# Kernel optimization log

Hardware: AMD Instinct MI355X
Metric: run time of the kernel (lower is better)

Reference implementation:

```python
import jax, jax.numpy as jnp
import numpy as np
from jax import lax

D = 1024
K = 3
LN_EPS = 1e-5


def setup_inputs() -> dict:
    key = jax.random.key(0)
    ks = jax.random.split(key, 8)
    B, T = 8, 4096
    x = jax.random.normal(ks[0], (B, T, D), dtype=jnp.float32)
    s = 1.0 / np.sqrt(D)
    in_proj_w = jax.random.uniform(ks[1], (D, 2 * D), jnp.float32, -s, s)
    in_proj_b = jax.random.uniform(ks[2], (2 * D,), jnp.float32, -s, s)
    conv_w = jax.random.uniform(ks[3], (D, 1, K), jnp.float32, -1.0 / np.sqrt(K), 1.0 / np.sqrt(K))
    conv_b = jax.random.uniform(ks[4], (D,), jnp.float32, -1.0 / np.sqrt(K), 1.0 / np.sqrt(K))
    logit_a = jnp.zeros((D,), jnp.float32)
    ssm_b = jnp.full((D,), 0.1, jnp.float32)
    ssm_c = jnp.ones((D,), jnp.float32)
    ssm_d = jnp.zeros((D,), jnp.float32)
    out_proj_w = jax.random.uniform(ks[5], (D, D), jnp.float32, -s, s)
    out_proj_b = jax.random.uniform(ks[6], (D,), jnp.float32, -s, s)
    ln_w = jnp.ones((D,), jnp.float32)
    ln_b = jnp.zeros((D,), jnp.float32)
    return {"x": x, "in_proj_w": in_proj_w, "in_proj_b": in_proj_b,
            "conv_w": conv_w, "conv_b": conv_b, "logit_a": logit_a,
            "ssm_b": ssm_b, "ssm_c": ssm_c, "ssm_d": ssm_d,
            "out_proj_w": out_proj_w, "out_proj_b": out_proj_b,
            "ln_w": ln_w, "ln_b": ln_b}


def _dwconv(v, conv_w, conv_b):
    # v: (B, T, D) -> depthwise conv1d, kernel K, 'same' padding
    vt = jnp.transpose(v, (0, 2, 1))  # (B, D, T)
    out = lax.conv_general_dilated(
        vt, conv_w, window_strides=(1,), padding=[(K // 2, K // 2)],
        dimension_numbers=("NCH", "OIH", "NCH"), feature_group_count=D)
    out = out + conv_b[None, :, None]
    return jnp.transpose(out, (0, 2, 1))  # (B, T, D)


def reference(x, in_proj_w, in_proj_b, conv_w, conv_b, logit_a,
              ssm_b, ssm_c, ssm_d, out_proj_w, out_proj_b, ln_w, ln_b):
    B, T, _ = x.shape
    residual = x
    uv = x @ in_proj_w + in_proj_b                      # (B, T, 2D)
    u, v = uv[..., :D], uv[..., D:]
    v = jax.nn.silu(v)
    v_local = _dwconv(v, conv_w, conv_b)                # (B, T, D)

    a = jax.nn.sigmoid(logit_a).astype(v_local.dtype)
    # diagonal LTI scan: h_t = a*h_{t-1} + b*u_t ; y_t = c*h_t + d*u_t
    def step(h, vt):
        h = a * h + ssm_b * vt
        return h, ssm_c * h + ssm_d * vt
    h0 = jnp.zeros((B, D), v_local.dtype)
    _, y_seq = lax.scan(step, h0, jnp.transpose(v_local, (1, 0, 2)))
    y_seq = jnp.transpose(y_seq, (1, 0, 2))             # (B, T, D)

    out = u * jax.nn.silu(y_seq)
    out = out @ out_proj_w + out_proj_b                 # dropout: eval mode (identity)
    h = out + residual
    mu = jnp.mean(h, axis=-1, keepdims=True)
    var = jnp.mean(jnp.square(h - mu), axis=-1, keepdims=True)
    return (h - mu) * lax.rsqrt(var + LN_EPS) * ln_w + ln_b
```

## Files before the change

kernel.cpp:

```cpp
#include <hip/hip_runtime.h>
#include <cstdint>
#include <cstddef>

#define D_DIM   1024
#define TWO_D   2048
#define B_DIM   8
#define T_DIM   4096
#define BT_DIM  (B_DIM*T_DIM)
#define LN_EPS  1e-5f
#define NCHUNK  128
#define CLEN    (T_DIM/NCHUNK)

typedef __attribute__((ext_vector_type(8))) short bf16x8;
typedef __attribute__((ext_vector_type(4))) float f32x4;

__device__ __forceinline__ float bf2f(unsigned short u){
  union { unsigned int i; float f; } c; c.i = ((unsigned int)u) << 16; return c.f;
}
__device__ __forceinline__ unsigned short f2bf(float f){
  union { float f; unsigned int i; } c; c.f = f;
  unsigned int x = c.i;
  return (unsigned short)((x + 0x7fffu + ((x >> 16) & 1u)) >> 16);
}
__device__ __forceinline__ float sigmoidf_(float x){ return 1.f/(1.f+__expf(-x)); }
__device__ __forceinline__ float siluf_(float x){ return x/(1.f+__expf(-x)); }


__global__ void cvt_f32_bf16(const float* __restrict__ in, unsigned short* __restrict__ out, int n){
  int i = (blockIdx.x*blockDim.x + threadIdx.x)*4;
  const int stride = gridDim.x*blockDim.x*4;
  for (; i + 3 < n; i += stride){
    float4 f = *(const float4*)(in + i);
    ushort4 o; o.x=f2bf(f.x); o.y=f2bf(f.y); o.z=f2bf(f.z); o.w=f2bf(f.w);
    *(ushort4*)(out + i) = o;
  }
}

__global__ void cvt_transpose(const float* __restrict__ W, unsigned short* __restrict__ Wt,
                              int rows, int cols){
  int i = blockIdx.x*blockDim.x + threadIdx.x;
  const int total = rows*cols;
  const int stride = gridDim.x*blockDim.x;
  for (; i < total; i += stride){
    int n = i / rows, k = i % rows;
    Wt[i] = f2bf(W[(size_t)k*cols + n]);
  }
}

template<int EPI>
__global__ __launch_bounds__(512, 2) void gemm256(
    const unsigned short* __restrict__ A,
    const unsigned short* __restrict__ Bt,
    const float* __restrict__ bias,
    const float* __restrict__ resid,
    unsigned short* __restrict__ outU,
    unsigned short* __restrict__ outV,
    float* __restrict__ outF,
    const int K, const int nbn)
{
  __shared__ __align__(16) unsigned short sA[2][2][8192];
  __shared__ __align__(16) unsigned short sB[2][2][8192];

#define BARRIER()   __builtin_amdgcn_s_barrier()
#define FENCE()     __builtin_amdgcn_sched_barrier(0)
#define WAIT_VM4()  do { asm volatile("s_waitcnt vmcnt(4)"); FENCE(); } while(0)
#define WAIT_VM0()  do { asm volatile("s_waitcnt vmcnt(0)"); FENCE(); } while(0)

  const int tid  = threadIdx.x;
  const int lane = tid & 63;
  const int wv   = tid >> 6;
  const int wr   = wv >> 2;
  const int wc   = wv & 3;
  const int fr   = lane & 15;
  const int fq   = lane >> 4;

  const int nwg = gridDim.x;
  const int cpx = nwg >> 3;
  const int wg  = (blockIdx.x & 7) * cpx + (blockIdx.x >> 3);
  const int bm = wg / nbn, bn = wg % nbn;

  const unsigned short* Ag = A  + (size_t)bm * 256 * K;
  const unsigned short* Bg = Bt + (size_t)bn * 256 * K;

  const int r0  = tid >> 2;
  const int r1  = 128 + r0;
  const int c0  = tid & 3;
  const int cs0 = c0 ^ ((r0 >> 1) & 3);
  const int cs1 = c0 ^ ((r1 >> 1) & 3);
  const int ld0 = tid * 8;
  const int ld1 = (512 + tid) * 8;

#define STAGE(ARR, srcp, kofs)                                                           \
  do {                                                                                   \
    __builtin_amdgcn_global_load_lds(                                                    \
      (const __attribute__((address_space(1))) void*)((srcp) + (size_t)r0*K + (kofs) + cs0*8), \
      (__attribute__((address_space(3))) void*)(&(ARR)[ld0]), 16, 0, 0);                 \
    __builtin_amdgcn_global_load_lds(                                                    \
      (const __attribute__((address_space(1))) void*)((srcp) + (size_t)r1*K + (kofs) + cs1*8), \
      (__attribute__((address_space(3))) void*)(&(ARR)[ld1]), 16, 0, 0);                 \
  } while(0)

  const int swz  = fq ^ ((fr >> 1) & 3);
  const int offA = (wr*128 + fr) * 32 + swz * 8;
  const int offB = (wc*64  + fr) * 32 + swz * 8;

  f32x4 acc[8][4];
#pragma unroll
  for (int i = 0; i < 8; ++i)
#pragma unroll
    for (int j = 0; j < 4; ++j) acc[i][j] = {0.f,0.f,0.f,0.f};

  bf16x8 afr[4], bfr[4];

#define PHASE(PAR, KH, MH, STAGE_STMT, TAIL_WAIT)                          \
  do {                                                                     \
    _Pragma("unroll")                                                      \
    for (int m2 = 0; m2 < 4; ++m2)                                         \
      afr[m2] = *(const bf16x8*)(&sA[PAR][KH][offA + ((MH)*4+m2)*512]);    \
    if ((MH) == 0) {                                                       \
      _Pragma("unroll")                                                    \
      for (int n2 = 0; n2 < 4; ++n2)                                       \
        bfr[n2] = *(const bf16x8*)(&sB[PAR][KH][offB + n2*512]);           \
    }                                                                      \
    STAGE_STMT;                                                            \
    BARRIER();                                                             \
    asm volatile("s_waitcnt lgkmcnt(0)");                                  \
    FENCE();                                                               \
    __builtin_amdgcn_s_setprio(1);                                         \
    _Pragma("unroll")                                                      \
    for (int n2 = 0; n2 < 4; ++n2)                                         \
      _Pragma("unroll")                                                    \
      for (int m2 = 0; m2 < 4; ++m2)                                       \
        acc[(MH)*4+m2][n2] = __builtin_amdgcn_mfma_f32_16x16x32_bf16(      \
            afr[m2], bfr[n2], acc[(MH)*4+m2][n2], 0, 0, 0);                \
    __builtin_amdgcn_s_setprio(0);                                         \
    TAIL_WAIT;                                                             \
    BARRIER();                                                             \
  } while(0)

  const int npairs = K >> 7;

  STAGE(sA[0][0], Ag, 0);
  STAGE(sB[0][0], Bg, 0);
  STAGE(sA[0][1], Ag, 32);
  STAGE(sB[0][1], Bg, 32);
  WAIT_VM4();
  BARRIER();

  for (int i = 0; i < npairs - 1; ++i){
    const int kbO = ((i << 1) + 1) << 6;
    const int kbE = ((i << 1) + 2) << 6;
    PHASE(0, 0, 0, STAGE(sA[1][0], Ag, kbO),      );
    PHASE(0, 0, 1, STAGE(sB[1][0], Bg, kbO),      WAIT_VM4());
    PHASE(0, 1, 0, STAGE(sA[1][1], Ag, kbO + 32), );
    PHASE(0, 1, 1, STAGE(sB[1][1], Bg, kbO + 32), WAIT_VM4());
    PHASE(1, 0, 0, STAGE(sA[0][0], Ag, kbE),      );
    PHASE(1, 0, 1, STAGE(sB[0][0], Bg, kbE),      WAIT_VM4());
    PHASE(1, 1, 0, STAGE(sA[0][1], Ag, kbE + 32), );
    PHASE(1, 1, 1, STAGE(sB[0][1], Bg, kbE + 32), WAIT_VM4());
  }
  PHASE(0, 0, 0, STAGE(sA[1][0], Ag, K - 64), );
  PHASE(0, 0, 1, STAGE(sB[1][0], Bg, K - 64), WAIT_VM4());
  PHASE(0, 1, 0, STAGE(sA[1][1], Ag, K - 32), );
  PHASE(0, 1, 1, STAGE(sB[1][1], Bg, K - 32), WAIT_VM4());
  PHASE(1, 0, 0, , );
  PHASE(1, 0, 1, , WAIT_VM0());
  PHASE(1, 1, 0, , );
  PHASE(1, 1, 1, , );

  const int nb = bn*256 + wc*64;
  const int mb = bm*256 + wr*128;
  float bsv[4];
#pragma unroll
  for (int ni = 0; ni < 4; ++ni) bsv[ni] = bias[nb + ni*16 + fr];

  if (EPI == 0){
    const bool isV = (nb >= D_DIM);
    unsigned short* dst = isV ? (outV + (nb - D_DIM)) : (outU + nb);
#pragma unroll
    for (int mi = 0; mi < 8; ++mi){
#pragma unroll
      for (int j = 0; j < 4; ++j){
        const int m = mb + mi*16 + fq*4 + j;
        unsigned short* row = dst + (size_t)m*D_DIM + fr;
#pragma unroll
        for (int ni = 0; ni < 4; ++ni){
          float cv = acc[mi][ni][j] + bsv[ni];
          row[ni*16] = f2bf(isV ? siluf_(cv) : cv);
        }
      }
    }
  } else {
#pragma unroll
    for (int mi = 0; mi < 8; ++mi){
#pragma unroll
      for (int j = 0; j < 4; ++j){
        const int m = mb + mi*16 + fq*4 + j;
        const float* rrow = resid + (size_t)m*D_DIM + nb + fr;
        float* orow = outF + (size_t)m*D_DIM + nb + fr;
#pragma unroll
        for (int ni = 0; ni < 4; ++ni)
          orow[ni*16] = acc[mi][ni][j] + bsv[ni] + rrow[ni*16];
      }
    }
  }
#undef PHASE
#undef STAGE
#undef BARRIER
#undef FENCE
#undef WAIT_VM4
#undef WAIT_VM0
}

__global__ __launch_bounds__(256) void scan_a(
    const unsigned short* __restrict__ v,
    const float* __restrict__ conv_w, const float* __restrict__ conv_b,
    const float* __restrict__ logit_a, const float* __restrict__ ssm_b,
    float* __restrict__ hend)
{
  const int b = blockIdx.x / NCHUNK;
  const int c = blockIdx.x % NCHUNK;
  const int d0 = threadIdx.x * 4;
  const int t0 = c * CLEN;
  const unsigned short* vb = v + (size_t)b * T_DIM * D_DIM;

  float w0[4], w1[4], w2[4], av[4], bv[4], cb[4];
#pragma unroll
  for (int i=0;i<4;i++){
    w0[i] = conv_w[(d0+i)*3+0];
    w1[i] = conv_w[(d0+i)*3+1];
    w2[i] = conv_w[(d0+i)*3+2];
    cb[i] = conv_b[d0+i];
    av[i] = sigmoidf_(logit_a[d0+i]);
    bv[i] = ssm_b[d0+i];
  }
  float vm1[4], v0[4], h[4] = {0.f,0.f,0.f,0.f};
  if (t0 == 0){
#pragma unroll
    for (int i=0;i<4;i++) vm1[i]=0.f;
  } else {
    ushort4 u = *(const ushort4*)(vb + (size_t)(t0-1)*D_DIM + d0);
    vm1[0]=bf2f(u.x); vm1[1]=bf2f(u.y); vm1[2]=bf2f(u.z); vm1[3]=bf2f(u.w);
  }
  {
    ushort4 u = *(const ushort4*)(vb + (size_t)t0*D_DIM + d0);
    v0[0]=bf2f(u.x); v0[1]=bf2f(u.y); v0[2]=bf2f(u.z); v0[3]=bf2f(u.w);
  }
#pragma unroll 8
  for (int t = t0; t < t0 + CLEN; ++t){
    float vp1[4];
    if (t + 1 < T_DIM){
      ushort4 u = *(const ushort4*)(vb + (size_t)(t+1)*D_DIM + d0);
      vp1[0]=bf2f(u.x); vp1[1]=bf2f(u.y); vp1[2]=bf2f(u.z); vp1[3]=bf2f(u.w);
    } else { vp1[0]=vp1[1]=vp1[2]=vp1[3]=0.f; }
#pragma unroll
    for (int i=0;i<4;i++){
      float vl = w0[i]*vm1[i] + w1[i]*v0[i] + w2[i]*vp1[i] + cb[i];
      h[i] = av[i]*h[i] + bv[i]*vl;
      vm1[i]=v0[i]; v0[i]=vp1[i];
    }
  }
  float* he = hend + ((size_t)b*NCHUNK + c)*D_DIM + d0;
#pragma unroll
  for (int i=0;i<4;i++) he[i] = h[i];
}

__global__ void scan_fix(const float* __restrict__ hend, const float* __restrict__ logit_a,
                         float* __restrict__ hinit)
{
  int idx = blockIdx.x*blockDim.x + threadIdx.x;
  if (idx >= B_DIM*D_DIM) return;
  const int b = idx / D_DIM, d = idx % D_DIM;
  const float a  = sigmoidf_(logit_a[d]);
  const float aL = __powf(a, (float)CLEN);
  float h = 0.f;
  for (int c = 0; c < NCHUNK; ++c){
    hinit[((size_t)b*NCHUNK + c)*D_DIM + d] = h;
    h = aL*h + hend[((size_t)b*NCHUNK + c)*D_DIM + d];
  }
}

__global__ __launch_bounds__(256) void scan_c(
    const unsigned short* __restrict__ v,
    const unsigned short* __restrict__ ubuf,
    const float* __restrict__ conv_w, const float* __restrict__ conv_b,
    const float* __restrict__ logit_a, const float* __restrict__ ssm_b,
    const float* __restrict__ ssm_c, const float* __restrict__ ssm_d,
    const float* __restrict__ hinit,
    unsigned short* __restrict__ gated)
{
  const int b = blockIdx.x / NCHUNK;
  const int c = blockIdx.x % NCHUNK;
  const int d0 = threadIdx.x * 4;
  const int t0 = c * CLEN;
  const unsigned short* vb = v    + (size_t)b * T_DIM * D_DIM;
  const unsigned short* ub = ubuf + (size_t)b * T_DIM * D_DIM;
  unsigned short* gb       = gated+ (size_t)b * T_DIM * D_DIM;

  float w0[4], w1[4], w2[4], av[4], bv[4], cb[4], scv[4], sdv[4], h[4];
#pragma unroll
  for (int i=0;i<4;i++){
    w0[i] = conv_w[(d0+i)*3+0];
    w1[i] = conv_w[(d0+i)*3+1];
    w2[i] = conv_w[(d0+i)*3+2];
    cb[i] = conv_b[d0+i];
    av[i] = sigmoidf_(logit_a[d0+i]);
    bv[i] = ssm_b[d0+i];
    scv[i] = ssm_c[d0+i];
    sdv[i] = ssm_d[d0+i];
    h[i] = hinit[((size_t)b*NCHUNK + c)*D_DIM + d0 + i];
  }
  float vm1[4], v0[4];
  if (t0 == 0){
#pragma unroll
    for (int i=0;i<4;i++) vm1[i]=0.f;
  } else {
    ushort4 u = *(const ushort4*)(vb + (size_t)(t0-1)*D_DIM + d0);
    vm1[0]=bf2f(u.x); vm1[1]=bf2f(u.y); vm1[2]=bf2f(u.z); vm1[3]=bf2f(u.w);
  }
  {
    ushort4 u = *(const ushort4*)(vb + (size_t)t0*D_DIM + d0);
    v0[0]=bf2f(u.x); v0[1]=bf2f(u.y); v0[2]=bf2f(u.z); v0[3]=bf2f(u.w);
  }
#pragma unroll 8
  for (int t = t0; t < t0 + CLEN; ++t){
    float vp1[4];
    if (t + 1 < T_DIM){
      ushort4 u = *(const ushort4*)(vb + (size_t)(t+1)*D_DIM + d0);
      vp1[0]=bf2f(u.x); vp1[1]=bf2f(u.y); vp1[2]=bf2f(u.z); vp1[3]=bf2f(u.w);
    } else { vp1[0]=vp1[1]=vp1[2]=vp1[3]=0.f; }
    ushort4 uu = *(const ushort4*)(ub + (size_t)t*D_DIM + d0);
    float uf[4] = { bf2f(uu.x), bf2f(uu.y), bf2f(uu.z), bf2f(uu.w) };
    ushort4 go;
    unsigned short gtmp[4];
#pragma unroll
    for (int i=0;i<4;i++){
      float vl = w0[i]*vm1[i] + w1[i]*v0[i] + w2[i]*vp1[i] + cb[i];
      h[i] = av[i]*h[i] + bv[i]*vl;
      float y = scv[i]*h[i] + sdv[i]*vl;
      gtmp[i] = f2bf(uf[i] * siluf_(y));
      vm1[i]=v0[i]; v0[i]=vp1[i];
    }
    go.x=gtmp[0]; go.y=gtmp[1]; go.z=gtmp[2]; go.w=gtmp[3];
    *(ushort4*)(gb + (size_t)t*D_DIM + d0) = go;
  }
}

__global__ __launch_bounds__(256) void ln_kernel(
    float* __restrict__ io, const float* __restrict__ lw, const float* __restrict__ lb)
{
  __shared__ float rs[4], rq[4];
  const int row = blockIdx.x;
  const int tid = threadIdx.x;
  float* p = io + (size_t)row * D_DIM;
  float4 x = *(const float4*)(p + tid*4);
  float s = x.x + x.y + x.z + x.w;
  float q = x.x*x.x + x.y*x.y + x.z*x.z + x.w*x.w;
#pragma unroll
  for (int off = 32; off > 0; off >>= 1){
    s += __shfl_down(s, off, 64);
    q += __shfl_down(q, off, 64);
  }
  const int wv = tid >> 6;
  if ((tid & 63) == 0){ rs[wv] = s; rq[wv] = q; }
  __syncthreads();
  const float ts = rs[0]+rs[1]+rs[2]+rs[3];
  const float tq = rq[0]+rq[1]+rq[2]+rq[3];
  const float mu  = ts * (1.f/(float)D_DIM);
  const float var = tq * (1.f/(float)D_DIM) - mu*mu;
  const float inv = rsqrtf(var + LN_EPS);
  const float4 w4 = *(const float4*)(lw + tid*4);
  const float4 b4 = *(const float4*)(lb + tid*4);
  float4 o;
  o.x = (x.x-mu)*inv*w4.x + b4.x;
  o.y = (x.y-mu)*inv*w4.y + b4.y;
  o.z = (x.z-mu)*inv*w4.z + b4.z;
  o.w = (x.w-mu)*inv*w4.w + b4.w;
  *(float4*)(p + tid*4) = o;
}

extern "C" void kernel_launch(void* const* d_in, const int* in_sizes, int n_in,
                              void* d_out, int out_size, void* d_ws, size_t ws_size,
                              hipStream_t stream)
{
  const float* x     = (const float*)d_in[0];
  const float* w1    = (const float*)d_in[1];
  const float* b1    = (const float*)d_in[2];
  const float* convw = (const float*)d_in[3];
  const float* convb = (const float*)d_in[4];
  const float* la    = (const float*)d_in[5];
  const float* sb    = (const float*)d_in[6];
  const float* sc    = (const float*)d_in[7];
  const float* sd    = (const float*)d_in[8];
  const float* w2    = (const float*)d_in[9];
  const float* b2    = (const float*)d_in[10];
  const float* lw    = (const float*)d_in[11];
  const float* lb    = (const float*)d_in[12];
  float* out = (float*)d_out;

  char* ws = (char*)d_ws;
  unsigned short* xb    = (unsigned short*)(ws + 0);
  unsigned short* ubf   = (unsigned short*)(ws + 67108864);
  unsigned short* vbf   = (unsigned short*)(ws + 134217728);
  unsigned short* w1t   = (unsigned short*)(ws + 201326592);
  unsigned short* w2t   = (unsigned short*)(ws + 205520896);
  float*          hend  = (float*)(ws + 207618048);
  float*          hinit = (float*)(ws + 211812352);

  cvt_f32_bf16<<<2048, 256, 0, stream>>>(x, xb, BT_DIM*D_DIM);
  cvt_transpose<<<2048, 256, 0, stream>>>(w1, w1t, D_DIM, TWO_D);
  cvt_transpose<<<1024, 256, 0, stream>>>(w2, w2t, D_DIM, D_DIM);

  gemm256<0><<<dim3((BT_DIM/256)*(TWO_D/256)), 512, 0, stream>>>(
      xb, w1t, b1, nullptr, ubf, vbf, nullptr, D_DIM, TWO_D/256);

  scan_a<<<B_DIM*NCHUNK, 256, 0, stream>>>(vbf, convw, convb, la, sb, hend);
  scan_fix<<<(B_DIM*D_DIM + 255)/256, 256, 0, stream>>>(hend, la, hinit);
  scan_c<<<B_DIM*NCHUNK, 256, 0, stream>>>(vbf, ubf, convw, convb, la, sb, sc, sd, hinit, xb);

  gemm256<1><<<dim3((BT_DIM/256)*(D_DIM/256)), 512, 0, stream>>>(
      xb, w2t, b2, x, nullptr, nullptr, out, D_DIM, D_DIM/256);

  ln_kernel<<<BT_DIM, 256, 0, stream>>>(out, lw, lb);
}
```

Measured before the change: 429.3 us.

## Double-buffer LDS fragment registers to overlap reads with MFMA in GEMM

```diff
diff --git a/kernel.cpp b/kernel.cpp
--- a/kernel.cpp
+++ b/kernel.cpp
@@ -63,8 +63,8 @@
 
 #define BARRIER()   __builtin_amdgcn_s_barrier()
 #define FENCE()     __builtin_amdgcn_sched_barrier(0)
-#define WAIT_VM4()  do { asm volatile("s_waitcnt vmcnt(4)"); FENCE(); } while(0)
-#define WAIT_VM0()  do { asm volatile("s_waitcnt vmcnt(0)"); FENCE(); } while(0)
+#define LGKM(N)     do { asm volatile("s_waitcnt lgkmcnt(" #N ")"); FENCE(); } while(0)
+#define VMW(N)      do { asm volatile("s_waitcnt vmcnt(" #N ")"); FENCE(); } while(0)
 
   const int tid  = threadIdx.x;
   const int lane = tid & 63;
@@ -90,7 +90,7 @@
   const int ld0 = tid * 8;
   const int ld1 = (512 + tid) * 8;
 
-#define STAGE(ARR, srcp, kofs)                                                           \
+#define STAGE1(ARR, srcp, kofs)                                                          \
   do {                                                                                   \
     __builtin_amdgcn_global_load_lds(                                                    \
       (const __attribute__((address_space(1))) void*)((srcp) + (size_t)r0*K + (kofs) + cs0*8), \
@@ -100,6 +100,14 @@
       (__attribute__((address_space(3))) void*)(&(ARR)[ld1]), 16, 0, 0);                 \
   } while(0)
 
+#define STAGE8(NP, kb)                 \
+  do {                                 \
+    STAGE1(sA[NP][0], Ag, (kb));       \
+    STAGE1(sB[NP][0], Bg, (kb));       \
+    STAGE1(sA[NP][1], Ag, (kb) + 32);  \
+    STAGE1(sB[NP][1], Bg, (kb) + 32);  \
+  } while(0)
+
   const int swz  = fq ^ ((fr >> 1) & 3);
   const int offA = (wr*128 + fr) * 32 + swz * 8;
   const int offB = (wc*64  + fr) * 32 + swz * 8;
@@ -110,63 +118,74 @@
 #pragma unroll
     for (int j = 0; j < 4; ++j) acc[i][j] = {0.f,0.f,0.f,0.f};
 
-  bf16x8 afr[4], bfr[4];
-
-#define PHASE(PAR, KH, MH, STAGE_STMT, TAIL_WAIT)                          \
+  bf16x8 afr[2][4], bfr[2][4];
+
+#define READ_A(SET, P, KH, MH)                                             \
+  do { _Pragma("unroll")                                                   \
+    for (int m2 = 0; m2 < 4; ++m2)                                         \
+      afr[SET][m2] = *(const bf16x8*)(&sA[P][KH][offA + ((MH)*4+m2)*512]); \
+  } while(0)
+#define READ_B(SET, P, KH)                                                 \
+  do { _Pragma("unroll")                                                   \
+    for (int n2 = 0; n2 < 4; ++n2)                                         \
+      bfr[SET][n2] = *(const bf16x8*)(&sB[P][KH][offB + n2*512]);          \
+  } while(0)
+#define MFMA16(AS, BS, ACB)                                                \
   do {                                                                     \
-    _Pragma("unroll")                                                      \
-    for (int m2 = 0; m2 < 4; ++m2)                                         \
-      afr[m2] = *(const bf16x8*)(&sA[PAR][KH][offA + ((MH)*4+m2)*512]);    \
-    if ((MH) == 0) {                                                       \
-      _Pragma("unroll")                                                    \
-      for (int n2 = 0; n2 < 4; ++n2)                                       \
-        bfr[n2] = *(const bf16x8*)(&sB[PAR][KH][offB + n2*512]);           \
-    }                                                                      \
-    STAGE_STMT;                                                            \
-    BARRIER();                                                             \
-    asm volatile("s_waitcnt lgkmcnt(0)");                                  \
-    FENCE();                                                               \
     __builtin_amdgcn_s_setprio(1);                                         \
     _Pragma("unroll")                                                      \
     for (int n2 = 0; n2 < 4; ++n2)                                         \
       _Pragma("unroll")                                                    \
       for (int m2 = 0; m2 < 4; ++m2)                                       \
-        acc[(MH)*4+m2][n2] = __builtin_amdgcn_mfma_f32_16x16x32_bf16(      \
-            afr[m2], bfr[n2], acc[(MH)*4+m2][n2], 0, 0, 0);                \
+        acc[(ACB)+m2][n2] = __builtin_amdgcn_mfma_f32_16x16x32_bf16(       \
+            afr[AS][m2], bfr[BS][n2], acc[(ACB)+m2][n2], 0, 0, 0);         \
     __builtin_amdgcn_s_setprio(0);                                         \
-    TAIL_WAIT;                                                             \
+  } while(0)
+
+#define TILE(P, NP, KB, LAST)                                              \
+  do {                                                                     \
+                 \
+    READ_A(1, P, 0, 1);                                                    \
+    if (!(LAST)) STAGE8(NP, KB);                                           \
+    FENCE(); BARRIER(); LGKM(4);                                           \
+    MFMA16(0, 0, 0);                                                       \
+    if (LAST) { VMW(0); } else { VMW(8); }              \
     BARRIER();                                                             \
+     \
+    READ_A(0, P, 1, 0); READ_B(1, P, 1);                                   \
+    FENCE(); BARRIER(); LGKM(8);                                           \
+    MFMA16(1, 0, 4);                                                       \
+    BARRIER();                                                             \
+                 \
+    READ_A(1, P, 1, 1);                                                    \
+    FENCE(); BARRIER(); LGKM(4);                                           \
+    MFMA16(0, 1, 0);                                                       \
+    if (!(LAST)) VMW(4);                              \
+    BARRIER();                                                             \
+     \
+    if (!(LAST)) { READ_A(0, NP, 0, 0); READ_B(0, NP, 0); }                \
+    FENCE(); BARRIER();                                                    \
+    if (LAST) { LGKM(0); } else { LGKM(8); }                               \
+    MFMA16(1, 1, 4);                                                       \
+    BARRIER();                                                             \
   } while(0)
 
   const int npairs = K >> 7;
 
-  STAGE(sA[0][0], Ag, 0);
-  STAGE(sB[0][0], Bg, 0);
-  STAGE(sA[0][1], Ag, 32);
-  STAGE(sB[0][1], Bg, 32);
-  WAIT_VM4();
+  STAGE8(0, 0);
+  VMW(4);
   BARRIER();
+  READ_A(0, 0, 0, 0); READ_B(0, 0, 0);
+  FENCE();
 
   for (int i = 0; i < npairs - 1; ++i){
     const int kbO = ((i << 1) + 1) << 6;
     const int kbE = ((i << 1) + 2) << 6;
-    PHASE(0, 0, 0, STAGE(sA[1][0], Ag, kbO),      );
-    PHASE(0, 0, 1, STAGE(sB[1][0], Bg, kbO),      WAIT_VM4());
-    PHASE(0, 1, 0, STAGE(sA[1][1], Ag, kbO + 32), );
-    PHASE(0, 1, 1, STAGE(sB[1][1], Bg, kbO + 32), WAIT_VM4());
-    PHASE(1, 0, 0, STAGE(sA[0][0], Ag, kbE),      );
-    PHASE(1, 0, 1, STAGE(sB[0][0], Bg, kbE),      WAIT_VM4());
-    PHASE(1, 1, 0, STAGE(sA[0][1], Ag, kbE + 32), );
-    PHASE(1, 1, 1, STAGE(sB[0][1], Bg, kbE + 32), WAIT_VM4());
-  }
-  PHASE(0, 0, 0, STAGE(sA[1][0], Ag, K - 64), );
-  PHASE(0, 0, 1, STAGE(sB[1][0], Bg, K - 64), WAIT_VM4());
-  PHASE(0, 1, 0, STAGE(sA[1][1], Ag, K - 32), );
-  PHASE(0, 1, 1, STAGE(sB[1][1], Bg, K - 32), WAIT_VM4());
-  PHASE(1, 0, 0, , );
-  PHASE(1, 0, 1, , WAIT_VM0());
-  PHASE(1, 1, 0, , );
-  PHASE(1, 1, 1, , );
+    TILE(0, 1, kbO, 0);
+    TILE(1, 0, kbE, 0);
+  }
+  TILE(0, 1, K - 64, 0);
+  TILE(1, 0, 0, 1);
 
   const int nb = bn*256 + wc*64;
   const int mb = bm*256 + wr*128;
@@ -204,12 +223,16 @@
       }
     }
   }
-#undef PHASE
-#undef STAGE
+#undef TILE
+#undef MFMA16
+#undef READ_A
+#undef READ_B
+#undef STAGE8
+#undef STAGE1
 #undef BARRIER
 #undef FENCE
-#undef WAIT_VM4
-#undef WAIT_VM0
+#undef LGKM
+#undef VMW
 }
 
 __global__ __launch_bounds__(256) void scan_a(
```

Measured after the change: 470.2 us. +9.5%, slower.

## Merge GEMM half-phases into full-K-slice phases and tile weight transpose via LDS

Applied to the files above, without the earlier changes.

```diff
diff --git a/kernel.cpp b/kernel.cpp
--- a/kernel.cpp
+++ b/kernel.cpp
@@ -36,15 +36,25 @@
   }
 }
 
-__global__ void cvt_transpose(const float* __restrict__ W, unsigned short* __restrict__ Wt,
-                              int rows, int cols){
-  int i = blockIdx.x*blockDim.x + threadIdx.x;
-  const int total = rows*cols;
-  const int stride = gridDim.x*blockDim.x;
-  for (; i < total; i += stride){
-    int n = i / rows, k = i % rows;
-    Wt[i] = f2bf(W[(size_t)k*cols + n]);
-  }
+__global__ __launch_bounds__(256) void cvt_transpose(
+    const float* __restrict__ W, unsigned short* __restrict__ Wt,
+    int rows, int cols)
+{
+  __shared__ float tile[32][33];
+  const int tx = threadIdx.x & 31;
+  const int ty = threadIdx.x >> 5;
+  const int tpc = cols >> 5;
+  const int bc = blockIdx.x % tpc;
+  const int br = blockIdx.x / tpc;
+  const int gc = bc*32 + tx;
+  const int gr = br*32;
+#pragma unroll
+  for (int i = 0; i < 32; i += 8)
+    tile[ty + i][tx] = W[(size_t)(gr + ty + i)*cols + gc];
+  __syncthreads();
+#pragma unroll
+  for (int i = 0; i < 32; i += 8)
+    Wt[(size_t)(bc*32 + ty + i)*rows + gr + tx] = f2bf(tile[tx][ty + i]);
 }
 
 template<int EPI>
@@ -110,29 +120,27 @@
 #pragma unroll
     for (int j = 0; j < 4; ++j) acc[i][j] = {0.f,0.f,0.f,0.f};
 
-  bf16x8 afr[4], bfr[4];
-
-#define PHASE(PAR, KH, MH, STAGE_STMT, TAIL_WAIT)                          \
+  bf16x8 afr[8], bfr[4];
+
+#define PHASE(PAR, KH, STAGE_STMT, TAIL_WAIT)                              \
   do {                                                                     \
     _Pragma("unroll")                                                      \
-    for (int m2 = 0; m2 < 4; ++m2)                                         \
-      afr[m2] = *(const bf16x8*)(&sA[PAR][KH][offA + ((MH)*4+m2)*512]);    \
-    if ((MH) == 0) {                                                       \
-      _Pragma("unroll")                                                    \
-      for (int n2 = 0; n2 < 4; ++n2)                                       \
-        bfr[n2] = *(const bf16x8*)(&sB[PAR][KH][offB + n2*512]);           \
-    }                                                                      \
+    for (int m2 = 0; m2 < 8; ++m2)                                         \
+      afr[m2] = *(const bf16x8*)(&sA[PAR][KH][offA + m2*512]);             \
+    _Pragma("unroll")                                                      \
+    for (int n2 = 0; n2 < 4; ++n2)                                         \
+      bfr[n2] = *(const bf16x8*)(&sB[PAR][KH][offB + n2*512]);             \
     STAGE_STMT;                                                            \
     BARRIER();                                                             \
     asm volatile("s_waitcnt lgkmcnt(0)");                                  \
     FENCE();                                                               \
     __builtin_amdgcn_s_setprio(1);                                         \
     _Pragma("unroll")                                                      \
-    for (int n2 = 0; n2 < 4; ++n2)                                         \
+    for (int m2 = 0; m2 < 8; ++m2)                                         \
       _Pragma("unroll")                                                    \
-      for (int m2 = 0; m2 < 4; ++m2)                                       \
-        acc[(MH)*4+m2][n2] = __builtin_amdgcn_mfma_f32_16x16x32_bf16(      \
-            afr[m2], bfr[n2], acc[(MH)*4+m2][n2], 0, 0, 0);                \
+      for (int n2 = 0; n2 < 4; ++n2)                                       \
+        acc[m2][n2] = __builtin_amdgcn_mfma_f32_16x16x32_bf16(             \
+            afr[m2], bfr[n2], acc[m2][n2], 0, 0, 0);                       \
     __builtin_amdgcn_s_setprio(0);                                         \
     TAIL_WAIT;                                                             \
     BARRIER();                                                             \
@@ -150,23 +158,15 @@
   for (int i = 0; i < npairs - 1; ++i){
     const int kbO = ((i << 1) + 1) << 6;
     const int kbE = ((i << 1) + 2) << 6;
-    PHASE(0, 0, 0, STAGE(sA[1][0], Ag, kbO),      );
-    PHASE(0, 0, 1, STAGE(sB[1][0], Bg, kbO),      WAIT_VM4());
-    PHASE(0, 1, 0, STAGE(sA[1][1], Ag, kbO + 32), );
-    PHASE(0, 1, 1, STAGE(sB[1][1], Bg, kbO + 32), WAIT_VM4());
-    PHASE(1, 0, 0, STAGE(sA[0][0], Ag, kbE),      );
-    PHASE(1, 0, 1, STAGE(sB[0][0], Bg, kbE),      WAIT_VM4());
-    PHASE(1, 1, 0, STAGE(sA[0][1], Ag, kbE + 32), );
-    PHASE(1, 1, 1, STAGE(sB[0][1], Bg, kbE + 32), WAIT_VM4());
-  }
-  PHASE(0, 0, 0, STAGE(sA[1][0], Ag, K - 64), );
-  PHASE(0, 0, 1, STAGE(sB[1][0], Bg, K - 64), WAIT_VM4());
-  PHASE(0, 1, 0, STAGE(sA[1][1], Ag, K - 32), );
-  PHASE(0, 1, 1, STAGE(sB[1][1], Bg, K - 32), WAIT_VM4());
-  PHASE(1, 0, 0, , );
-  PHASE(1, 0, 1, , WAIT_VM0());
-  PHASE(1, 1, 0, , );
-  PHASE(1, 1, 1, , );
+    PHASE(0, 0, { STAGE(sA[1][0], Ag, kbO);      STAGE(sB[1][0], Bg, kbO);      }, WAIT_VM4());
+    PHASE(0, 1, { STAGE(sA[1][1], Ag, kbO + 32); STAGE(sB[1][1], Bg, kbO + 32); }, WAIT_VM4());
+    PHASE(1, 0, { STAGE(sA[0][0], Ag, kbE);      STAGE(sB[0][0], Bg, kbE);      }, WAIT_VM4());
+    PHASE(1, 1, { STAGE(sA[0][1], Ag, kbE + 32); STAGE(sB[0][1], Bg, kbE + 32); }, WAIT_VM4());
+  }
+  PHASE(0, 0, { STAGE(sA[1][0], Ag, K - 64); STAGE(sB[1][0], Bg, K - 64); }, WAIT_VM4());
+  PHASE(0, 1, { STAGE(sA[1][1], Ag, K - 32); STAGE(sB[1][1], Bg, K - 32); }, WAIT_VM4());
+  PHASE(1, 0, , WAIT_VM0());
+  PHASE(1, 1, , );
 
   const int nb = bn*256 + wc*64;
   const int mb = bm*256 + wr*128;
@@ -408,8 +408,8 @@
   float*          hinit = (float*)(ws + 211812352);
 
   cvt_f32_bf16<<<2048, 256, 0, stream>>>(x, xb, BT_DIM*D_DIM);
-  cvt_transpose<<<2048, 256, 0, stream>>>(w1, w1t, D_DIM, TWO_D);
-  cvt_transpose<<<1024, 256, 0, stream>>>(w2, w2t, D_DIM, D_DIM);
+  cvt_transpose<<<(D_DIM/32)*(TWO_D/32), 256, 0, stream>>>(w1, w1t, D_DIM, TWO_D);
+  cvt_transpose<<<(D_DIM/32)*(D_DIM/32), 256, 0, stream>>>(w2, w2t, D_DIM, D_DIM);
 
   gemm256<0><<<dim3((BT_DIM/256)*(TWO_D/256)), 512, 0, stream>>>(
       xb, w1t, b1, nullptr, ubf, vbf, nullptr, D_DIM, TWO_D/256);
```

Result: no change. 426.9 us (-0.6%).
